# Kernel tuning notes

Measured on AMD Instinct MI355X. Metric: run time of the kernel, lower is better.

The kernel has to match this reference:

```python
import jax, jax.numpy as jnp
import numpy as np

D_MODEL = 1024
NUM_HEAD = 16
HEAD_DIM = D_MODEL // NUM_HEAD
S, B = 2048, 2


def setup_inputs() -> dict:
    key = jax.random.key(0)
    ks = jax.random.split(key, 8)
    q = jax.random.normal(ks[0], (S, B, D_MODEL), dtype=jnp.float32)
    k = jax.random.normal(ks[1], (S, B, D_MODEL), dtype=jnp.float32)
    v = jax.random.normal(ks[2], (S, B, D_MODEL), dtype=jnp.float32)
    attn_mask = jnp.zeros((S, S), dtype=jnp.float32)
    # xavier_uniform_ bound for square (D,D) linear: sqrt(6/(D+D))
    bound = float(np.sqrt(6.0 / (D_MODEL + D_MODEL)))
    def w(k_):
        return jax.random.uniform(k_, (D_MODEL, D_MODEL), jnp.float32, -bound, bound)
    Wq, Wk, Wv, Wo = w(ks[3]), w(ks[4]), w(ks[5]), w(ks[6])
    zb = jnp.zeros((D_MODEL,), jnp.float32)
    return {"q": q, "k": k, "v": v, "attn_mask": attn_mask,
            "Wq": Wq, "bq": zb, "Wk": Wk, "bk": zb,
            "Wv": Wv, "bv": zb, "Wo": Wo, "bo": zb}


def reference(q, k, v, attn_mask, Wq, bq, Wk, bk, Wv, bv, Wo, bo):
    s, b, d = q.shape
    h, hd = NUM_HEAD, HEAD_DIM
    # QKV projections (torch Linear: x @ W.T + b)
    qp = q @ Wq.T + bq  # (S,B,D)
    kp = k @ Wk.T + bk
    vp = v @ Wv.T + bv
    # (S,B,H,Dh) -> permute(2,1,0,3) -> (H,B,S,Dh)
    qh = jnp.transpose(qp.reshape(s, b, h, hd), (2, 1, 0, 3))
    kh = jnp.transpose(kp.reshape(s, b, h, hd), (2, 1, 0, 3))
    vh = jnp.transpose(vp.reshape(s, b, h, hd), (2, 1, 0, 3))
    scores = jnp.einsum('hbqd,hbkd->hbqk', qh, kh) / jnp.sqrt(jnp.float32(hd))
    scores = scores + attn_mask  # additive mask broadcast over (H,B,*,*)
    weights = jax.nn.softmax(scores, axis=-1)
    out = jnp.einsum('hbqk,hbkd->hbqd', weights, vh)  # (H,B,S,Dh)
    # Faithful to original: raw contiguous view (H,B,S,Dh) -> (S,B,D)
    out = out.reshape(s, b, d)
    return out @ Wo.T + bo
```

## Files before the change

kernel.cpp:

```cpp
#include <hip/hip_runtime.h>
#include <hip/hip_bf16.h>
#include <cstdint>
#include <cstddef>

typedef unsigned short u16;
typedef short bf16x8 __attribute__((ext_vector_type(8)));
typedef short bf16x4 __attribute__((ext_vector_type(4)));
typedef unsigned short u16x8 __attribute__((ext_vector_type(8)));
typedef unsigned short u16x4 __attribute__((ext_vector_type(4)));
typedef float f32x4 __attribute__((ext_vector_type(4)));

#define S_LEN 2048
#define BATCH 2
#define DM 1024
#define NHEAD 16
#define HDIM 64
#define MROWS (S_LEN * BATCH)
#define LOG2E 1.44269504088896340736f
#define KSPLIT 4
#define SPAN (S_LEN / KSPLIT)
#define NROWS (NHEAD * BATCH * S_LEN)

__device__ __forceinline__ u16 f32_to_bf16(float f) {
  union { float f; uint32_t u; } v; v.f = f;
  uint32_t u = v.u;
  u += 0x7FFFu + ((u >> 16) & 1u);
  return (u16)(u >> 16);
}
__device__ __forceinline__ u16 cvt_bf16(float f) {
  __hip_bfloat16 h = __float2bfloat16(f);
  return *reinterpret_cast<u16*>(&h);
}
__device__ __forceinline__ float bf2f(u16 x) {
  union { float f; uint32_t u; } v; v.u = ((uint32_t)x) << 16; return v.f;
}

__device__ __forceinline__ void gload_lds16(const void* g, void* l) {
  __builtin_amdgcn_global_load_lds(
      (const __attribute__((address_space(1))) void*)g,
      (__attribute__((address_space(3))) void*)l, 16, 0, 0);
}

__device__ __forceinline__ bf16x4 tr_read(const void* lp) {
  bf16x4 d;
  auto p = (const __attribute__((address_space(3))) short*)lp;
  asm volatile("ds_read_b64_tr_b16 %0, %1" : "=v"(d) : "v"(p));
  return d;
}

#if __has_builtin(__builtin_amdgcn_mfma_f32_16x16x16_bf16)
#define MFMA16(a, b, c) __builtin_amdgcn_mfma_f32_16x16x16_bf16(a, b, c, 0, 0, 0)
#elif __has_builtin(__builtin_amdgcn_mfma_f32_16x16x16bf16_1k)
#define MFMA16(a, b, c) __builtin_amdgcn_mfma_f32_16x16x16bf16_1k(a, b, c, 0, 0, 0)
#else
__device__ __forceinline__ f32x4 mfma16_asm(bf16x4 a, bf16x4 b, f32x4 c) {
  f32x4 d;
  asm volatile("v_mfma_f32_16x16x16_bf16 %0, %1, %2, %3\n\ts_nop 7\n\ts_nop 7"
               : "=&v"(d) : "v"(a), "v"(b), "v"(c));
  return d;
}
#define MFMA16(a, b, c) mfma16_asm(a, b, c)
#endif

__global__ void cast4_f32_bf16(const float* __restrict__ s0, u16* __restrict__ d0,
                               const float* __restrict__ s1, u16* __restrict__ d1,
                               const float* __restrict__ s2, u16* __restrict__ d2,
                               const float* __restrict__ s3, u16* __restrict__ d3,
                               int n8) {
  const int which = blockIdx.y;
  const float* src = which == 0 ? s0 : which == 1 ? s1 : which == 2 ? s2 : s3;
  u16* dst = which == 0 ? d0 : which == 1 ? d1 : which == 2 ? d2 : d3;
  int i = blockIdx.x * blockDim.x + threadIdx.x;
  const int stride = gridDim.x * blockDim.x;
  for (; i < n8; i += stride) {
    const float4* s = (const float4*)(src + (size_t)i * 8);
    float4 a = s[0];
    float4 b = s[1];
    u16x8 o;
    o[0] = f32_to_bf16(a.x); o[1] = f32_to_bf16(a.y);
    o[2] = f32_to_bf16(a.z); o[3] = f32_to_bf16(a.w);
    o[4] = f32_to_bf16(b.x); o[5] = f32_to_bf16(b.y);
    o[6] = f32_to_bf16(b.z); o[7] = f32_to_bf16(b.w);
    *(u16x8*)(dst + (size_t)i * 8) = o;
  }
}

__global__ void scale_f32(const float* __restrict__ src, float* __restrict__ dst,
                          float sc, int n4) {
  int i = blockIdx.x * blockDim.x + threadIdx.x;
  const int stride = gridDim.x * blockDim.x;
  for (; i < n4; i += stride) {
    float4 a = *(const float4*)(src + (size_t)i * 4);
    a.x *= sc; a.y *= sc; a.z *= sc; a.w *= sc;
    *(float4*)(dst + (size_t)i * 4) = a;
  }
}

template <int MODE>
__device__ __forceinline__ void gemm_body(
    const u16* __restrict__ A, const u16* __restrict__ Bw, const float* __restrict__ bias,
    float* __restrict__ outF, u16* __restrict__ outP, float oscale,
    u16* As, u16* Bs)
{
  const int K = DM, N = DM;
  const int tid = threadIdx.x;
  const int wave = tid >> 6, lane = tid & 63;
  const int l15 = lane & 15, l4 = lane >> 4;
  const int wr = wave >> 1, wc = wave & 1;
  const int rowBase = blockIdx.y * 128, colBase = blockIdx.x * 64;

  f32x4 acc[4][2];
#pragma unroll
  for (int m = 0; m < 4; ++m)
#pragma unroll
    for (int n = 0; n < 2; ++n) acc[m][n] = (f32x4){0.f, 0.f, 0.f, 0.f};

  for (int k0 = 0; k0 < K; k0 += 32) {
#pragma unroll
    for (int c = 0; c < 2; ++c) {
      const int ldsbyte = wave * 2048 + c * 1024;
      const int elt = (ldsbyte >> 1) + lane * 8;
      const int r = elt >> 5, cc = elt & 31;
      gload_lds16(A + (size_t)(rowBase + r) * K + k0 + cc, (char*)As + ldsbyte);
    }
    {
      const int ldsbyte = wave * 1024;
      const int elt = (ldsbyte >> 1) + lane * 8;
      const int r = elt >> 5, cc = elt & 31;
      gload_lds16(Bw + (size_t)(colBase + r) * K + k0 + cc, (char*)Bs + ldsbyte);
    }
    __syncthreads();

    bf16x8 af[4], bfr[2];
#pragma unroll
    for (int m = 0; m < 4; ++m)
      af[m] = *(const bf16x8*)&As[(wr * 64 + m * 16 + l15) * 32 + 8 * l4];
#pragma unroll
    for (int n = 0; n < 2; ++n)
      bfr[n] = *(const bf16x8*)&Bs[(wc * 32 + n * 16 + l15) * 32 + 8 * l4];
#pragma unroll
    for (int m = 0; m < 4; ++m)
#pragma unroll
      for (int n = 0; n < 2; ++n)
        acc[m][n] = __builtin_amdgcn_mfma_f32_16x16x32_bf16(af[m], bfr[n], acc[m][n], 0, 0, 0);
    __syncthreads();
  }

#pragma unroll
  for (int m = 0; m < 4; ++m)
#pragma unroll
    for (int n = 0; n < 2; ++n)
#pragma unroll
      for (int j = 0; j < 4; ++j) {
        const int row = rowBase + wr * 64 + m * 16 + 4 * l4 + j;
        const int col = colBase + wc * 32 + n * 16 + l15;
        const float vv = (acc[m][n][j] + bias[col]) * oscale;
        if (MODE == 0) {
          const int s = row >> 1, b = row & 1, h = col >> 6, dh = col & 63;
          outP[((size_t)(h * BATCH + b) * S_LEN + s) * HDIM + dh] = f32_to_bf16(vv);
        } else {
          outF[(size_t)row * N + col] = vv;
        }
      }
}

__global__ __launch_bounds__(256) void gemm_qkv(
    const u16* __restrict__ Aq, const u16* __restrict__ Ak, const u16* __restrict__ Av,
    const u16* __restrict__ Wq, const u16* __restrict__ Wk, const u16* __restrict__ Wv,
    const float* __restrict__ bq, const float* __restrict__ bk, const float* __restrict__ bv,
    u16* __restrict__ Oq, u16* __restrict__ Ok, u16* __restrict__ Ov, float qscale)
{
  __shared__ u16 As[128 * 32];
  __shared__ u16 Bs[64 * 32];
  const int z = blockIdx.z;
  const u16* A  = z == 0 ? Aq : z == 1 ? Ak : Av;
  const u16* W  = z == 0 ? Wq : z == 1 ? Wk : Wv;
  const float* b = z == 0 ? bq : z == 1 ? bk : bv;
  u16* O = z == 0 ? Oq : z == 1 ? Ok : Ov;
  const float sc = z == 0 ? qscale : 1.f;
  gemm_body<0>(A, W, b, nullptr, O, sc, As, Bs);
}

__global__ __launch_bounds__(256) void gemm_out(
    const u16* __restrict__ A, const u16* __restrict__ W, const float* __restrict__ bias,
    float* __restrict__ outF)
{
  __shared__ u16 As[128 * 32];
  __shared__ u16 Bs[64 * 32];
  gemm_body<1>(A, W, bias, outF, nullptr, 1.f, As, Bs);
}

__device__ __forceinline__ void stageK_swz(const u16* __restrict__ Kp, int kt, u16* dst, int tid) {
#pragma unroll
  for (int h = 0; h < 2; ++h) {
    const int c = tid + 256 * h;
    const int r = c >> 3, x = c & 7;
    gload_lds16(Kp + (size_t)(kt + r) * HDIM + (x ^ (r & 7)) * 8, (char*)dst + 16 * c);
  }
}
__device__ __forceinline__ void stageV(const u16* __restrict__ Vp, int kt, u16* dst, int tid) {
#pragma unroll
  for (int h = 0; h < 2; ++h) {
    const int c = tid + 256 * h;
    const int key = 4 * ((c >> 3) & 15) + ((c >> 1) & 3);
    const int dh  = 16 * (c >> 7) + 8 * (c & 1);
    gload_lds16(Vp + (size_t)(kt + key) * HDIM + dh, (char*)dst + 16 * c);
  }
}

__global__ __launch_bounds__(256, 4) void flash_attn(
    const u16* __restrict__ Qh, const u16* __restrict__ Kh, const u16* __restrict__ Vh,
    const float* __restrict__ maskf, u16* __restrict__ Opart, float2* __restrict__ mlp)
{
  const int hb = blockIdx.y;
  const int z  = blockIdx.z;
  const int qb = blockIdx.x * 128;
  const int kbase = z * SPAN;
  const u16* Qp = Qh + (size_t)hb * S_LEN * HDIM;
  const u16* Kp = Kh + (size_t)hb * S_LEN * HDIM + (size_t)kbase * HDIM;
  const u16* Vp = Vh + (size_t)hb * S_LEN * HDIM + (size_t)kbase * HDIM;
  const float* mp = maskf + kbase;
  const int tid = threadIdx.x;
  const int wave = tid >> 6, lane = tid & 63;
  const int l15 = lane & 15, l4 = lane >> 4;
  const int qrow0 = qb + wave * 32 + l15;
  const int qrow1 = qrow0 + 16;

  __shared__ u16 Klds[2][4096];
  __shared__ u16 Vlds[2][4096];

  bf16x8 bq[2][2];
  bq[0][0] = *(const bf16x8*)&Qp[(size_t)qrow0 * HDIM + 8 * l4];
  bq[0][1] = *(const bf16x8*)&Qp[(size_t)qrow0 * HDIM + 32 + 8 * l4];
  bq[1][0] = *(const bf16x8*)&Qp[(size_t)qrow1 * HDIM + 8 * l4];
  bq[1][1] = *(const bf16x8*)&Qp[(size_t)qrow1 * HDIM + 32 + 8 * l4];

  stageK_swz(Kp, 0, &Klds[0][0], tid);
  stageV(Vp, 0, &Vlds[0][0], tid);

  float m_run[2] = {-1e30f, -1e30f}, l_run[2] = {0.f, 0.f};
  f32x4 oacc[2][4];
#pragma unroll
  for (int f = 0; f < 2; ++f)
#pragma unroll
    for (int D = 0; D < 4; ++D) oacc[f][D] = (f32x4){0.f, 0.f, 0.f, 0.f};

  __syncthreads();

  for (int kt = 0; kt < SPAN; kt += 64) {
    const int cur = (kt >> 6) & 1;
    if (kt + 64 < SPAN) {
      stageK_swz(Kp, kt + 64, &Klds[cur ^ 1][0], tid);
      stageV(Vp, kt + 64, &Vlds[cur ^ 1][0], tid);
    }
    float4 mc[2][4];
#pragma unroll
    for (int kb = 0; kb < 4; ++kb) {
      mc[0][kb] = *(const float4*)&mp[(size_t)qrow0 * S_LEN + kt + 16 * kb + 4 * l4];
      mc[1][kb] = *(const float4*)&mp[(size_t)qrow1 * S_LEN + kt + 16 * kb + 4 * l4];
    }

    bf16x4 pb[2][4];
#pragma unroll
    for (int f = 0; f < 2; ++f) {
      f32x4 st[4];
#pragma unroll
      for (int kb = 0; kb < 4; ++kb) {
        const int r = 16 * kb + l15;
        const int s0 = (l4 ^ (l15 & 7)) * 8;
        const int s1 = ((l4 + 4) ^ (l15 & 7)) * 8;
        bf16x8 k0 = *(const bf16x8*)&Klds[cur][r * 64 + s0];
        bf16x8 k1 = *(const bf16x8*)&Klds[cur][r * 64 + s1];
        f32x4 zz = (f32x4){0.f, 0.f, 0.f, 0.f};
        zz = __builtin_amdgcn_mfma_f32_16x16x32_bf16(k0, bq[f][0], zz, 0, 0, 0);
        zz = __builtin_amdgcn_mfma_f32_16x16x32_bf16(k1, bq[f][1], zz, 0, 0, 0);
        st[kb] = zz;
      }
      float p[16];
#pragma unroll
      for (int kb = 0; kb < 4; ++kb) {
        p[4 * kb + 0] = st[kb][0] + mc[f][kb].x;
        p[4 * kb + 1] = st[kb][1] + mc[f][kb].y;
        p[4 * kb + 2] = st[kb][2] + mc[f][kb].z;
        p[4 * kb + 3] = st[kb][3] + mc[f][kb].w;
      }

      float t0 = fmaxf(fmaxf(p[0], p[1]), fmaxf(p[2], p[3]));
      float t1 = fmaxf(fmaxf(p[4], p[5]), fmaxf(p[6], p[7]));
      float t2 = fmaxf(fmaxf(p[8], p[9]), fmaxf(p[10], p[11]));
      float t3 = fmaxf(fmaxf(p[12], p[13]), fmaxf(p[14], p[15]));
      float tm = fmaxf(fmaxf(t0, t1), fmaxf(t2, t3));
      tm = fmaxf(tm, __shfl_xor(tm, 16));
      tm = fmaxf(tm, __shfl_xor(tm, 32));

      if (!__all(tm - m_run[f] <= 11.0f)) {
        const float mn_ = fmaxf(m_run[f], tm);
        const float fac = exp2f(m_run[f] - mn_);
#pragma unroll
        for (int D = 0; D < 4; ++D)
#pragma unroll
          for (int j = 0; j < 4; ++j) oacc[f][D][j] *= fac;
        l_run[f] *= fac;
        m_run[f] = mn_;
      }

      float rs = 0.f;
#pragma unroll
      for (int kb = 0; kb < 4; ++kb)
#pragma unroll
        for (int e = 0; e < 4; ++e) {
          const float pe = exp2f(p[4 * kb + e] - m_run[f]);
          rs += pe;
          pb[f][kb][e] = (short)cvt_bf16(pe);
        }
      rs += __shfl_xor(rs, 16);
      rs += __shfl_xor(rs, 32);
      l_run[f] += rs;
    }

    const char* vb = (const char*)&Vlds[cur][0] + 8 * lane;
#pragma unroll
    for (int g = 0; g < 2; ++g) {
      bf16x4 va[2][4];
#pragma unroll
      for (int D = 0; D < 2; ++D)
#pragma unroll
        for (int kb = 0; kb < 4; ++kb)
          va[D][kb] = tr_read(vb + 2048 * (2 * g + D) + 512 * kb);
      asm volatile("s_waitcnt lgkmcnt(0)" ::: "memory");
      __builtin_amdgcn_sched_barrier(0);
#pragma unroll
      for (int D = 0; D < 2; ++D)
#pragma unroll
        for (int kb = 0; kb < 4; ++kb) {
          oacc[0][2 * g + D] = MFMA16(va[D][kb], pb[0][kb], oacc[0][2 * g + D]);
          oacc[1][2 * g + D] = MFMA16(va[D][kb], pb[1][kb], oacc[1][2 * g + D]);
        }
    }

    __syncthreads();
  }

  u16* Oz = Opart + (size_t)z * NROWS * HDIM;
#pragma unroll
  for (int f = 0; f < 2; ++f) {
    const float inv = 1.0f / l_run[f];
    const int qr = f == 0 ? qrow0 : qrow1;
    const size_t row = (size_t)hb * S_LEN + qr;
#pragma unroll
    for (int D = 0; D < 4; ++D) {
      u16x4 ov;
#pragma unroll
      for (int j = 0; j < 4; ++j) ov[j] = f32_to_bf16(oacc[f][D][j] * inv);
      *(u16x4*)&Oz[row * HDIM + 16 * D + 4 * l4] = ov;
    }
    if (l4 == 0) mlp[(size_t)z * NROWS + row] = make_float2(m_run[f], l_run[f]);
  }
}

__global__ __launch_bounds__(256) void fa_combine(
    const u16* __restrict__ Opart, const float2* __restrict__ mlp, u16* __restrict__ Ob)
{
  const int idx = blockIdx.x * blockDim.x + threadIdx.x;
  const int row = idx >> 4, c = idx & 15;
  float2 ml[KSPLIT];
  float m = -1e30f;
#pragma unroll
  for (int zz = 0; zz < KSPLIT; ++zz) {
    ml[zz] = mlp[(size_t)zz * NROWS + row];
    m = fmaxf(m, ml[zz].x);
  }
  float w[KSPLIT], tot = 0.f;
#pragma unroll
  for (int zz = 0; zz < KSPLIT; ++zz) {
    w[zz] = exp2f(ml[zz].x - m) * ml[zz].y;
    tot += w[zz];
  }
  const float inv = 1.f / tot;
  const size_t off = (size_t)row * HDIM + 4 * c;
  float a0 = 0.f, a1 = 0.f, a2 = 0.f, a3 = 0.f;
#pragma unroll
  for (int zz = 0; zz < KSPLIT; ++zz) {
    const u16x4 o = *(const u16x4*)&Opart[(size_t)zz * NROWS * HDIM + off];
    const float wz = w[zz] * inv;
    a0 += wz * bf2f((u16)o[0]);
    a1 += wz * bf2f((u16)o[1]);
    a2 += wz * bf2f((u16)o[2]);
    a3 += wz * bf2f((u16)o[3]);
  }
  u16x4 o;
  o[0] = f32_to_bf16(a0); o[1] = f32_to_bf16(a1);
  o[2] = f32_to_bf16(a2); o[3] = f32_to_bf16(a3);
  *(u16x4*)&Ob[off] = o;
}

extern "C" void kernel_launch(void* const* d_in, const int* in_sizes, int n_in,
                              void* d_out, int out_size, void* d_ws, size_t ws_size,
                              hipStream_t stream) {
  const float* q    = (const float*)d_in[0];
  const float* k    = (const float*)d_in[1];
  const float* v    = (const float*)d_in[2];
  const float* mask = (const float*)d_in[3];
  const float* Wq   = (const float*)d_in[4];
  const float* bq   = (const float*)d_in[5];
  const float* Wk   = (const float*)d_in[6];
  const float* bk   = (const float*)d_in[7];
  const float* Wv   = (const float*)d_in[8];
  const float* bv   = (const float*)d_in[9];
  const float* Wo   = (const float*)d_in[10];
  const float* bo   = (const float*)d_in[11];
  float* out = (float*)d_out;

  char* ws = (char*)d_ws;
  const size_t MB = 1024 * 1024;
  u16*  Qh    = (u16*)(ws + 0 * MB);
  u16*  Kh    = (u16*)(ws + 8 * MB);
  u16*  Vh    = (u16*)(ws + 16 * MB);
  float* maskf = (float*)(ws + 24 * MB);
  u16*  wob   = (u16*)(ws + 40 * MB);
  u16*  Ob    = (u16*)(ws + 42 * MB);
  u16*  qb_   = (u16*)(ws + 50 * MB);
  u16*  kb_   = (u16*)(ws + 58 * MB);
  u16*  vb_   = (u16*)(ws + 66 * MB);
  u16*  wqb   = (u16*)(ws + 74 * MB);
  u16*  wkb   = (u16*)(ws + 76 * MB);
  u16*  wvb   = (u16*)(ws + 78 * MB);
  u16*  Opart = (u16*)(ws + 50 * MB);
  float2* mlp = (float2*)(ws + 82 * MB);

  const int n8_t = MROWS * DM / 8;
  const int n8_w = DM * DM / 8;
  cast4_f32_bf16<<<dim3(1024, 3), 256, 0, stream>>>(
      q, qb_, k, kb_, v, vb_, q, qb_, n8_t);
  cast4_f32_bf16<<<dim3(256, 4), 256, 0, stream>>>(
      Wq, wqb, Wk, wkb, Wv, wvb, Wo, wob, n8_w);
  scale_f32<<<2048, 256, 0, stream>>>(mask, maskf, LOG2E, S_LEN * S_LEN / 4);

  const float qscale = 0.125f * LOG2E;
  gemm_qkv<<<dim3(DM / 64, MROWS / 128, 3), 256, 0, stream>>>(
      qb_, kb_, vb_, wqb, wkb, wvb, bq, bk, bv, Qh, Kh, Vh, qscale);

  flash_attn<<<dim3(S_LEN / 128, NHEAD * BATCH, KSPLIT), 256, 0, stream>>>(
      Qh, Kh, Vh, maskf, Opart, mlp);
  fa_combine<<<NROWS * 16 / 256, 256, 0, stream>>>(Opart, mlp, Ob);

  gemm_out<<<dim3(DM / 64, MROWS / 128), 256, 0, stream>>>(Ob, wob, bo, out);
}
```

Before: 220.1 us.

## Store additive mask as bf16, fold its scaling into the cast kernel, halve KSPLIT

After: 184.8 us. 1.19x faster.

```diff
diff --git a/kernel.cpp b/kernel.cpp
--- a/kernel.cpp
+++ b/kernel.cpp
@@ -17,7 +17,7 @@
 #define HDIM 64
 #define MROWS (S_LEN * BATCH)
 #define LOG2E 1.44269504088896340736f
-#define KSPLIT 4
+#define KSPLIT 2
 #define SPAN (S_LEN / KSPLIT)
 #define NROWS (NHEAD * BATCH * S_LEN)
 
@@ -66,10 +66,11 @@
                                const float* __restrict__ s1, u16* __restrict__ d1,
                                const float* __restrict__ s2, u16* __restrict__ d2,
                                const float* __restrict__ s3, u16* __restrict__ d3,
-                               int n8) {
+                               float4 scales, int n8) {
   const int which = blockIdx.y;
   const float* src = which == 0 ? s0 : which == 1 ? s1 : which == 2 ? s2 : s3;
   u16* dst = which == 0 ? d0 : which == 1 ? d1 : which == 2 ? d2 : d3;
+  const float sc = which == 0 ? scales.x : which == 1 ? scales.y : which == 2 ? scales.z : scales.w;
   int i = blockIdx.x * blockDim.x + threadIdx.x;
   const int stride = gridDim.x * blockDim.x;
   for (; i < n8; i += stride) {
@@ -77,22 +78,11 @@
     float4 a = s[0];
     float4 b = s[1];
     u16x8 o;
-    o[0] = f32_to_bf16(a.x); o[1] = f32_to_bf16(a.y);
-    o[2] = f32_to_bf16(a.z); o[3] = f32_to_bf16(a.w);
-    o[4] = f32_to_bf16(b.x); o[5] = f32_to_bf16(b.y);
-    o[6] = f32_to_bf16(b.z); o[7] = f32_to_bf16(b.w);
+    o[0] = f32_to_bf16(a.x * sc); o[1] = f32_to_bf16(a.y * sc);
+    o[2] = f32_to_bf16(a.z * sc); o[3] = f32_to_bf16(a.w * sc);
+    o[4] = f32_to_bf16(b.x * sc); o[5] = f32_to_bf16(b.y * sc);
+    o[6] = f32_to_bf16(b.z * sc); o[7] = f32_to_bf16(b.w * sc);
     *(u16x8*)(dst + (size_t)i * 8) = o;
-  }
-}
-
-__global__ void scale_f32(const float* __restrict__ src, float* __restrict__ dst,
-                          float sc, int n4) {
-  int i = blockIdx.x * blockDim.x + threadIdx.x;
-  const int stride = gridDim.x * blockDim.x;
-  for (; i < n4; i += stride) {
-    float4 a = *(const float4*)(src + (size_t)i * 4);
-    a.x *= sc; a.y *= sc; a.z *= sc; a.w *= sc;
-    *(float4*)(dst + (size_t)i * 4) = a;
   }
 }
 
@@ -210,7 +200,7 @@
 
 __global__ __launch_bounds__(256, 4) void flash_attn(
     const u16* __restrict__ Qh, const u16* __restrict__ Kh, const u16* __restrict__ Vh,
-    const float* __restrict__ maskf, u16* __restrict__ Opart, float2* __restrict__ mlp)
+    const u16* __restrict__ maskb, u16* __restrict__ Opart, float2* __restrict__ mlp)
 {
   const int hb = blockIdx.y;
   const int z  = blockIdx.z;
@@ -219,7 +209,7 @@
   const u16* Qp = Qh + (size_t)hb * S_LEN * HDIM;
   const u16* Kp = Kh + (size_t)hb * S_LEN * HDIM + (size_t)kbase * HDIM;
   const u16* Vp = Vh + (size_t)hb * S_LEN * HDIM + (size_t)kbase * HDIM;
-  const float* mp = maskf + kbase;
+  const u16* mp = maskb + kbase;
   const int tid = threadIdx.x;
   const int wave = tid >> 6, lane = tid & 63;
   const int l15 = lane & 15, l4 = lane >> 4;
@@ -253,11 +243,11 @@
       stageK_swz(Kp, kt + 64, &Klds[cur ^ 1][0], tid);
       stageV(Vp, kt + 64, &Vlds[cur ^ 1][0], tid);
     }
-    float4 mc[2][4];
+    u16x4 mc[2][4];
 #pragma unroll
     for (int kb = 0; kb < 4; ++kb) {
-      mc[0][kb] = *(const float4*)&mp[(size_t)qrow0 * S_LEN + kt + 16 * kb + 4 * l4];
-      mc[1][kb] = *(const float4*)&mp[(size_t)qrow1 * S_LEN + kt + 16 * kb + 4 * l4];
+      mc[0][kb] = *(const u16x4*)&mp[(size_t)qrow0 * S_LEN + kt + 16 * kb + 4 * l4];
+      mc[1][kb] = *(const u16x4*)&mp[(size_t)qrow1 * S_LEN + kt + 16 * kb + 4 * l4];
     }
 
     bf16x4 pb[2][4];
@@ -278,12 +268,10 @@
       }
       float p[16];
 #pragma unroll
-      for (int kb = 0; kb < 4; ++kb) {
-        p[4 * kb + 0] = st[kb][0] + mc[f][kb].x;
-        p[4 * kb + 1] = st[kb][1] + mc[f][kb].y;
-        p[4 * kb + 2] = st[kb][2] + mc[f][kb].z;
-        p[4 * kb + 3] = st[kb][3] + mc[f][kb].w;
-      }
+      for (int kb = 0; kb < 4; ++kb)
+#pragma unroll
+        for (int j = 0; j < 4; ++j)
+          p[4 * kb + j] = st[kb][j] + bf2f((u16)mc[f][kb][j]);
 
       float t0 = fmaxf(fmaxf(p[0], p[1]), fmaxf(p[2], p[3]));
       float t1 = fmaxf(fmaxf(p[4], p[5]), fmaxf(p[6], p[7]));
@@ -416,32 +404,33 @@
   u16*  Qh    = (u16*)(ws + 0 * MB);
   u16*  Kh    = (u16*)(ws + 8 * MB);
   u16*  Vh    = (u16*)(ws + 16 * MB);
-  float* maskf = (float*)(ws + 24 * MB);
-  u16*  wob   = (u16*)(ws + 40 * MB);
-  u16*  Ob    = (u16*)(ws + 42 * MB);
-  u16*  qb_   = (u16*)(ws + 50 * MB);
-  u16*  kb_   = (u16*)(ws + 58 * MB);
-  u16*  vb_   = (u16*)(ws + 66 * MB);
-  u16*  wqb   = (u16*)(ws + 74 * MB);
-  u16*  wkb   = (u16*)(ws + 76 * MB);
-  u16*  wvb   = (u16*)(ws + 78 * MB);
-  u16*  Opart = (u16*)(ws + 50 * MB);
-  float2* mlp = (float2*)(ws + 82 * MB);
+  u16*  maskb = (u16*)(ws + 24 * MB);
+  u16*  wob   = (u16*)(ws + 32 * MB);
+  u16*  Ob    = (u16*)(ws + 34 * MB);
+  u16*  qb_   = (u16*)(ws + 42 * MB);
+  u16*  kb_   = (u16*)(ws + 50 * MB);
+  u16*  vb_   = (u16*)(ws + 58 * MB);
+  u16*  wqb   = (u16*)(ws + 66 * MB);
+  u16*  wkb   = (u16*)(ws + 68 * MB);
+  u16*  wvb   = (u16*)(ws + 70 * MB);
+  u16*  Opart = (u16*)(ws + 42 * MB);
+  float2* mlp = (float2*)(ws + 58 * MB);
 
   const int n8_t = MROWS * DM / 8;
   const int n8_w = DM * DM / 8;
-  cast4_f32_bf16<<<dim3(1024, 3), 256, 0, stream>>>(
-      q, qb_, k, kb_, v, vb_, q, qb_, n8_t);
+  cast4_f32_bf16<<<dim3(1024, 4), 256, 0, stream>>>(
+      q, qb_, k, kb_, v, vb_, mask, maskb,
+      make_float4(1.f, 1.f, 1.f, LOG2E), n8_t);
   cast4_f32_bf16<<<dim3(256, 4), 256, 0, stream>>>(
-      Wq, wqb, Wk, wkb, Wv, wvb, Wo, wob, n8_w);
-  scale_f32<<<2048, 256, 0, stream>>>(mask, maskf, LOG2E, S_LEN * S_LEN / 4);
+      Wq, wqb, Wk, wkb, Wv, wvb, Wo, wob,
+      make_float4(1.f, 1.f, 1.f, 1.f), n8_w);
 
   const float qscale = 0.125f * LOG2E;
   gemm_qkv<<<dim3(DM / 64, MROWS / 128, 3), 256, 0, stream>>>(
       qb_, kb_, vb_, wqb, wkb, wvb, bq, bk, bv, Qh, Kh, Vh, qscale);
 
   flash_attn<<<dim3(S_LEN / 128, NHEAD * BATCH, KSPLIT), 256, 0, stream>>>(
-      Qh, Kh, Vh, maskf, Opart, mlp);
+      Qh, Kh, Vh, maskb, Opart, mlp);
   fa_combine<<<NROWS * 16 / 256, 256, 0, stream>>>(Opart, mlp, Ob);
 
   gemm_out<<<dim3(DM / 64, MROWS / 128), 256, 0, stream>>>(Ob, wob, bo, out);
```
